# Kernel tuning notes

Measured on AMD Instinct MI355X. Metric: run time of the kernel, lower is better.

The kernel has to match this reference:

```python
import jax, jax.numpy as jnp
import numpy as np


def setup_inputs() -> dict:
    key = jax.random.key(0)
    k1, k2, k3 = jax.random.split(key, 3)
    N, K, QB = 8192, 8192, 128
    x = jax.random.normal(k1, (K,), dtype=jnp.float16)
    # packed int4 weights: two nibbles per byte, stored as int32 in [0, 256)
    packed_w = jax.random.randint(k2, (N, K // 2), 0, 256, dtype=jnp.int32)
    # per-(row, quant-block) FP16 scales, small positive values
    scales = (jax.random.uniform(k3, (N, K // QB), dtype=jnp.float32) * 0.05 + 0.001).astype(jnp.float16)
    return {"x": x, "packed_w": packed_w, "scales": scales, "qblock_size": QB}


def reference(x, packed_w, scales, qblock_size):
    # Unpack int4 weights: low nibble -> even k, high nibble -> odd k, offset-8.
    N, half_K = packed_w.shape
    K = half_K * 2
    lo = (packed_w & 0x0F) - 8          # [N, K/2]
    hi = ((packed_w >> 4) & 0x0F) - 8   # [N, K/2]
    w_int = jnp.stack([lo, hi], axis=-1).reshape(N, K).astype(jnp.float32)

    # Factored-scale GEMV (mirrors kernel: integer dot per quant-block, then one
    # multiply by the block scale).
    blocks = K // qblock_size
    wb = w_int.reshape(N, blocks, qblock_size)                 # [N, B, Q]
    xb = x.astype(jnp.float32).reshape(blocks, qblock_size)    # [B, Q]
    partial = jnp.einsum('nbq,bq->nb', wb, xb)                 # [N, B]
    out = jnp.sum(partial * scales.astype(jnp.float32), axis=1)
    return out.astype(jnp.float16)
```

## Files before the change

### kernel.cpp

```cpp
#include <hip/hip_runtime.h>


#define WAVES_PER_BLOCK 4

__global__ __launch_bounds__(256, 4)
void eoq_gemv_kernel(const float* __restrict__ x,
                     const int* __restrict__ packed_w,
                     const float* __restrict__ scales,
                     float* __restrict__ out,
                     int N, int halfK, int itMask, int sShift, int blocksPerRow)
{
    const int lane = threadIdx.x & 63;
    const int wave = threadIdx.x >> 6;
    const int row  = blockIdx.x * WAVES_PER_BLOCK + wave;
    if (row >= N) return;

    const int4*   __restrict__ w4p =
        reinterpret_cast<const int4*>(packed_w + (size_t)row * halfK);
    const float4* __restrict__ x4p = reinterpret_cast<const float4*>(x);
    const float*  __restrict__ srow = scales + (size_t)row * (size_t)blocksPerRow;

    const int iters = itMask + 1;
    const int phase = row & itMask;

    float acc = 0.f;

    #pragma unroll 4
    for (int t = 0; t < iters; ++t) {
        const int it = (t + phase) & itMask;
        const int j4 = (it << 6) + lane;
        const int4   w4 = w4p[j4];
        const float4 xa = x4p[2 * j4];
        const float4 xb = x4p[2 * j4 + 1];
        const float  s  = srow[j4 >> sShift];

        const unsigned w0 = (unsigned)w4.x;
        const unsigned w1 = (unsigned)w4.y;
        const unsigned w2 = (unsigned)w4.z;
        const unsigned w3 = (unsigned)w4.w;

        float part = 0.f;
        part = fmaf((float)(int)(w0 & 0xFu) - 8.f, xa.x, part);
        part = fmaf((float)(int)(w0 >> 4)   - 8.f, xa.y, part);
        part = fmaf((float)(int)(w1 & 0xFu) - 8.f, xa.z, part);
        part = fmaf((float)(int)(w1 >> 4)   - 8.f, xa.w, part);
        part = fmaf((float)(int)(w2 & 0xFu) - 8.f, xb.x, part);
        part = fmaf((float)(int)(w2 >> 4)   - 8.f, xb.y, part);
        part = fmaf((float)(int)(w3 & 0xFu) - 8.f, xb.z, part);
        part = fmaf((float)(int)(w3 >> 4)   - 8.f, xb.w, part);
        acc = fmaf(s, part, acc);
    }

    #pragma unroll
    for (int off = 32; off > 0; off >>= 1)
        acc += __shfl_down(acc, off, 64);

    if (lane == 0) out[row] = acc;
}

extern "C" void kernel_launch(void* const* d_in, const int* in_sizes, int n_in,
                              void* d_out, int out_size, void* d_ws, size_t ws_size,
                              hipStream_t stream) {
    const float* x      = (const float*)d_in[0];
    const int*   pw     = (const int*)d_in[1];
    const float* scales = (const float*)d_in[2];
    float*       out    = (float*)d_out;

    const int K     = in_sizes[0];
    const int halfK = K >> 1;
    const int N     = in_sizes[1] / halfK;
    const int blocksPerRow = in_sizes[2] / N;

    const int qhalf = halfK / blocksPerRow;
    int qhalfShift = 0;
    while ((1 << qhalfShift) < qhalf) ++qhalfShift;
    const int sShift = qhalfShift - 2;

    const int iters = halfK >> 8;
    const int itMask = iters - 1;

    dim3 grid((N + WAVES_PER_BLOCK - 1) / WAVES_PER_BLOCK), block(256);
    eoq_gemv_kernel<<<grid, block, 0, stream>>>(x, pw, scales, out,
                                                N, halfK, itMask, sShift, blocksPerRow);
}
```

Before: 202.5 us.

## Compute four rows per wave to reuse activation loads

Each wavefront now accumulates four output rows and shares each loaded x vector across them, using four times fewer blocks. This reduces redundant activation loads and per-row overhead and exposes more independent weight loads per iteration. In exchange, fewer waves are launched and the occupancy hint is lowered, and the per-row iteration phase stagger is dropped, which may change memory channel contention.

```diff
diff --git a/kernel.cpp b/kernel.cpp
--- a/kernel.cpp
+++ b/kernel.cpp
@@ -1,61 +1,70 @@
 #include <hip/hip_runtime.h>
 
 
-#define WAVES_PER_BLOCK 4
+#define ROWS_PER_WAVE 4
 
-__global__ __launch_bounds__(256, 4)
+__global__ __launch_bounds__(256, 2)
 void eoq_gemv_kernel(const float* __restrict__ x,
                      const int* __restrict__ packed_w,
                      const float* __restrict__ scales,
                      float* __restrict__ out,
-                     int N, int halfK, int itMask, int sShift, int blocksPerRow)
+                     int N, int halfK, int iters, int sShift, int blocksPerRow)
 {
     const int lane = threadIdx.x & 63;
     const int wave = threadIdx.x >> 6;
-    const int row  = blockIdx.x * WAVES_PER_BLOCK + wave;
-    if (row >= N) return;
+    const int row0 = (blockIdx.x * 4 + wave) * ROWS_PER_WAVE;
+    if (row0 >= N) return;
 
-    const int4*   __restrict__ w4p =
-        reinterpret_cast<const int4*>(packed_w + (size_t)row * halfK);
     const float4* __restrict__ x4p = reinterpret_cast<const float4*>(x);
-    const float*  __restrict__ srow = scales + (size_t)row * (size_t)blocksPerRow;
 
-    const int iters = itMask + 1;
-    const int phase = row & itMask;
+    const int4* w4p[ROWS_PER_WAVE];
+    const float* srow[ROWS_PER_WAVE];
+    #pragma unroll
+    for (int r = 0; r < ROWS_PER_WAVE; ++r) {
+        w4p[r]  = reinterpret_cast<const int4*>(packed_w + (size_t)(row0 + r) * halfK);
+        srow[r] = scales + (size_t)(row0 + r) * blocksPerRow;
+    }
 
-    float acc = 0.f;
+    float acc[ROWS_PER_WAVE] = {0.f, 0.f, 0.f, 0.f};
 
-    #pragma unroll 4
-    for (int t = 0; t < iters; ++t) {
-        const int it = (t + phase) & itMask;
+    #pragma unroll 2
+    for (int it = 0; it < iters; ++it) {
         const int j4 = (it << 6) + lane;
-        const int4   w4 = w4p[j4];
         const float4 xa = x4p[2 * j4];
         const float4 xb = x4p[2 * j4 + 1];
-        const float  s  = srow[j4 >> sShift];
+        const int    sIdx = j4 >> sShift;
 
-        const unsigned w0 = (unsigned)w4.x;
-        const unsigned w1 = (unsigned)w4.y;
-        const unsigned w2 = (unsigned)w4.z;
-        const unsigned w3 = (unsigned)w4.w;
+        #pragma unroll
+        for (int r = 0; r < ROWS_PER_WAVE; ++r) {
+            const int4  w4 = w4p[r][j4];
+            const float s  = srow[r][sIdx];
 
-        float part = 0.f;
-        part = fmaf((float)(int)(w0 & 0xFu) - 8.f, xa.x, part);
-        part = fmaf((float)(int)(w0 >> 4)   - 8.f, xa.y, part);
-        part = fmaf((float)(int)(w1 & 0xFu) - 8.f, xa.z, part);
-        part = fmaf((float)(int)(w1 >> 4)   - 8.f, xa.w, part);
-        part = fmaf((float)(int)(w2 & 0xFu) - 8.f, xb.x, part);
-        part = fmaf((float)(int)(w2 >> 4)   - 8.f, xb.y, part);
-        part = fmaf((float)(int)(w3 & 0xFu) - 8.f, xb.z, part);
-        part = fmaf((float)(int)(w3 >> 4)   - 8.f, xb.w, part);
-        acc = fmaf(s, part, acc);
+            const unsigned w0 = (unsigned)w4.x;
+            const unsigned w1 = (unsigned)w4.y;
+            const unsigned w2 = (unsigned)w4.z;
+            const unsigned w3 = (unsigned)w4.w;
+
+            float part = 0.f;
+            part = fmaf((float)(int)(w0 & 0xFu) - 8.f, xa.x, part);
+            part = fmaf((float)(int)(w0 >> 4)   - 8.f, xa.y, part);
+            part = fmaf((float)(int)(w1 & 0xFu) - 8.f, xa.z, part);
+            part = fmaf((float)(int)(w1 >> 4)   - 8.f, xa.w, part);
+            part = fmaf((float)(int)(w2 & 0xFu) - 8.f, xb.x, part);
+            part = fmaf((float)(int)(w2 >> 4)   - 8.f, xb.y, part);
+            part = fmaf((float)(int)(w3 & 0xFu) - 8.f, xb.z, part);
+            part = fmaf((float)(int)(w3 >> 4)   - 8.f, xb.w, part);
+            acc[r] = fmaf(s, part, acc[r]);
+        }
     }
 
     #pragma unroll
-    for (int off = 32; off > 0; off >>= 1)
-        acc += __shfl_down(acc, off, 64);
-
-    if (lane == 0) out[row] = acc;
+    for (int r = 0; r < ROWS_PER_WAVE; ++r) {
+        float a = acc[r];
+        #pragma unroll
+        for (int off = 32; off > 0; off >>= 1)
+            a += __shfl_down(a, off, 64);
+        if (lane == 0 && row0 + r < N) out[row0 + r] = a;
+    }
 }
 
 extern "C" void kernel_launch(void* const* d_in, const int* in_sizes, int n_in,
@@ -77,9 +86,9 @@
     const int sShift = qhalfShift - 2;
 
     const int iters = halfK >> 8;
-    const int itMask = iters - 1;
 
-    dim3 grid((N + WAVES_PER_BLOCK - 1) / WAVES_PER_BLOCK), block(256);
+    const int rowsPerBlock = 4 * ROWS_PER_WAVE;
+    dim3 grid((N + rowsPerBlock - 1) / rowsPerBlock), block(256);
     eoq_gemv_kernel<<<grid, block, 0, stream>>>(x, pw, scales, out,
-                                                N, halfK, itMask, sShift, blocksPerRow);
+                                                N, halfK, iters, sShift, blocksPerRow);
 }
```

After: 197.1 us. 2.7% less time.

## Software-pipeline weight/x loads with register ring buffer and shuffle-broadcast scales

Applied to the files above, without the earlier changes.

Adds a four-deep register prefetch ring so the weight and x loads for iteration t+4 are issued while iteration t is computed. Removes the per-row phase rotation of the K traversal. When a row has at most 64 scale blocks, each lane loads one scale up front and the loop broadcasts it with a wavefront shuffle instead of a global load per iteration. The prefetch buffers raise register pressure, which may cut occupancy under the existing launch bounds. Dropping the phase rotation means all rows read x in the same order, which may concentrate cache traffic.

```diff
diff --git a/kernel.cpp b/kernel.cpp
--- a/kernel.cpp
+++ b/kernel.cpp
@@ -1,38 +1,59 @@
 #include <hip/hip_runtime.h>
 
 
-#define WAVES_PER_BLOCK 4
+#define PF 4
 
+template<bool SHFL_SCALES>
 __global__ __launch_bounds__(256, 4)
 void eoq_gemv_kernel(const float* __restrict__ x,
                      const int* __restrict__ packed_w,
                      const float* __restrict__ scales,
                      float* __restrict__ out,
-                     int N, int halfK, int itMask, int sShift, int blocksPerRow)
+                     int N, int halfK, int iters, int sShift, int blocksPerRow)
 {
     const int lane = threadIdx.x & 63;
     const int wave = threadIdx.x >> 6;
-    const int row  = blockIdx.x * WAVES_PER_BLOCK + wave;
+    const int row  = blockIdx.x * 4 + wave;
     if (row >= N) return;
 
     const int4*   __restrict__ w4p =
         reinterpret_cast<const int4*>(packed_w + (size_t)row * halfK);
     const float4* __restrict__ x4p = reinterpret_cast<const float4*>(x);
-    const float*  __restrict__ srow = scales + (size_t)row * (size_t)blocksPerRow;
+    const float*  __restrict__ srow = scales + (size_t)row * blocksPerRow;
 
-    const int iters = itMask + 1;
-    const int phase = row & itMask;
+    float sAll = 0.f;
+    if (SHFL_SCALES) {
+        sAll = (lane < blocksPerRow) ? srow[lane] : 0.f;
+    }
+
+    int4   wbuf[PF];
+    float4 xabuf[PF];
+    float4 xbbuf[PF];
+
+    #pragma unroll
+    for (int p = 0; p < PF; ++p) {
+        const int c  = (p < iters) ? p : (iters - 1);
+        const int j4 = (c << 6) + lane;
+        wbuf[p]  = w4p[j4];
+        xabuf[p] = x4p[2 * j4];
+        xbbuf[p] = x4p[2 * j4 + 1];
+    }
 
     float acc = 0.f;
 
     #pragma unroll 4
     for (int t = 0; t < iters; ++t) {
-        const int it = (t + phase) & itMask;
-        const int j4 = (it << 6) + lane;
-        const int4   w4 = w4p[j4];
-        const float4 xa = x4p[2 * j4];
-        const float4 xb = x4p[2 * j4 + 1];
-        const float  s  = srow[j4 >> sShift];
+        const int slot = t & (PF - 1);
+        const int4   w4 = wbuf[slot];
+        const float4 xa = xabuf[slot];
+        const float4 xb = xbbuf[slot];
+
+        float s;
+        if (SHFL_SCALES) {
+            s = __shfl(sAll, ((t << 6) + lane) >> sShift, 64);
+        } else {
+            s = srow[((t << 6) + lane) >> sShift];
+        }
 
         const unsigned w0 = (unsigned)w4.x;
         const unsigned w1 = (unsigned)w4.y;
@@ -49,6 +70,12 @@
         part = fmaf((float)(int)(w3 & 0xFu) - 8.f, xb.z, part);
         part = fmaf((float)(int)(w3 >> 4)   - 8.f, xb.w, part);
         acc = fmaf(s, part, acc);
+
+        const int nc = (t + PF < iters) ? (t + PF) : (iters - 1);
+        const int j4 = (nc << 6) + lane;
+        wbuf[slot]  = w4p[j4];
+        xabuf[slot] = x4p[2 * j4];
+        xbbuf[slot] = x4p[2 * j4 + 1];
     }
 
     #pragma unroll
@@ -77,9 +104,13 @@
     const int sShift = qhalfShift - 2;
 
     const int iters = halfK >> 8;
-    const int itMask = iters - 1;
 
-    dim3 grid((N + WAVES_PER_BLOCK - 1) / WAVES_PER_BLOCK), block(256);
-    eoq_gemv_kernel<<<grid, block, 0, stream>>>(x, pw, scales, out,
-                                                N, halfK, itMask, sShift, blocksPerRow);
+    dim3 grid((N + 3) / 4), block(256);
+    if (blocksPerRow <= 64) {
+        eoq_gemv_kernel<true><<<grid, block, 0, stream>>>(
+            x, pw, scales, out, N, halfK, iters, sShift, blocksPerRow);
+    } else {
+        eoq_gemv_kernel<false><<<grid, block, 0, stream>>>(
+            x, pw, scales, out, N, halfK, iters, sShift, blocksPerRow);
+    }
 }
```

New measurement: 289.4 us. 1.43x slower.

## Add register-pipelined GEMV kernel with prefetch depth and shuffled scales

Applied to the files above, without the earlier changes.

Adds a templated kernel for the 16-iteration case that prefetches weights and x into an 8-deep register ring buffer, fully unrolls the loop, and loads all row scales once then distributes them via wave shuffles. The aim is to raise memory-level parallelism and hide load latency in the bandwidth-bound GEMV. It removes the per-row phase rotation and keeps a generic fallback kernel. The cost is higher register usage, which may limit occupancy.

```diff
diff --git a/kernel.cpp b/kernel.cpp
--- a/kernel.cpp
+++ b/kernel.cpp
@@ -1,33 +1,103 @@
 #include <hip/hip_runtime.h>
 
 
-#define WAVES_PER_BLOCK 4
+#define DEPTH 8
 
+template<int ITERS>
 __global__ __launch_bounds__(256, 4)
-void eoq_gemv_kernel(const float* __restrict__ x,
-                     const int* __restrict__ packed_w,
-                     const float* __restrict__ scales,
-                     float* __restrict__ out,
-                     int N, int halfK, int itMask, int sShift, int blocksPerRow)
+void eoq_gemv_pipe(const float* __restrict__ x,
+                   const int* __restrict__ packed_w,
+                   const float* __restrict__ scales,
+                   float* __restrict__ out,
+                   int N, int halfK, int sShift, int blocksPerRow)
 {
     const int lane = threadIdx.x & 63;
     const int wave = threadIdx.x >> 6;
-    const int row  = blockIdx.x * WAVES_PER_BLOCK + wave;
+    const int row  = blockIdx.x * 4 + wave;
     if (row >= N) return;
 
     const int4*   __restrict__ w4p =
         reinterpret_cast<const int4*>(packed_w + (size_t)row * halfK);
     const float4* __restrict__ x4p = reinterpret_cast<const float4*>(x);
-    const float*  __restrict__ srow = scales + (size_t)row * (size_t)blocksPerRow;
+    const float*  __restrict__ srow = scales + (size_t)row * blocksPerRow;
 
-    const int iters = itMask + 1;
-    const int phase = row & itMask;
+    const float sAll = (lane < blocksPerRow) ? srow[lane] : 0.f;
+
+    int4   wr[DEPTH];
+    float4 xar[DEPTH];
+    float4 xbr[DEPTH];
+
+    #pragma unroll
+    for (int p = 0; p < DEPTH; ++p) {
+        const int j4 = (p << 6) + lane;
+        wr[p]  = w4p[j4];
+        xar[p] = x4p[2 * j4];
+        xbr[p] = x4p[2 * j4 + 1];
+    }
 
     float acc = 0.f;
 
-    #pragma unroll 4
-    for (int t = 0; t < iters; ++t) {
-        const int it = (t + phase) & itMask;
+    #pragma unroll
+    for (int t = 0; t < ITERS; ++t) {
+        const int slot = t & (DEPTH - 1);
+
+        const int4   w4 = wr[slot];
+        const float4 xa = xar[slot];
+        const float4 xb = xbr[slot];
+
+        if (t + DEPTH < ITERS) {
+            const int j4 = ((t + DEPTH) << 6) + lane;
+            wr[slot]  = w4p[j4];
+            xar[slot] = x4p[2 * j4];
+            xbr[slot] = x4p[2 * j4 + 1];
+        }
+
+        const float s = __shfl(sAll, ((t << 6) + lane) >> sShift, 64);
+
+        const unsigned w0 = (unsigned)w4.x;
+        const unsigned w1 = (unsigned)w4.y;
+        const unsigned w2 = (unsigned)w4.z;
+        const unsigned w3 = (unsigned)w4.w;
+
+        float part = 0.f;
+        part = fmaf((float)(int)(w0 & 0xFu) - 8.f, xa.x, part);
+        part = fmaf((float)(int)(w0 >> 4)   - 8.f, xa.y, part);
+        part = fmaf((float)(int)(w1 & 0xFu) - 8.f, xa.z, part);
+        part = fmaf((float)(int)(w1 >> 4)   - 8.f, xa.w, part);
+        part = fmaf((float)(int)(w2 & 0xFu) - 8.f, xb.x, part);
+        part = fmaf((float)(int)(w2 >> 4)   - 8.f, xb.y, part);
+        part = fmaf((float)(int)(w3 & 0xFu) - 8.f, xb.z, part);
+        part = fmaf((float)(int)(w3 >> 4)   - 8.f, xb.w, part);
+        acc = fmaf(s, part, acc);
+    }
+
+    #pragma unroll
+    for (int off = 32; off > 0; off >>= 1)
+        acc += __shfl_down(acc, off, 64);
+
+    if (lane == 0) out[row] = acc;
+}
+
+__global__ __launch_bounds__(256, 2)
+void eoq_gemv_generic(const float* __restrict__ x,
+                      const int* __restrict__ packed_w,
+                      const float* __restrict__ scales,
+                      float* __restrict__ out,
+                      int N, int halfK, int iters, int sShift, int blocksPerRow)
+{
+    const int lane = threadIdx.x & 63;
+    const int wave = threadIdx.x >> 6;
+    const int row  = blockIdx.x * 4 + wave;
+    if (row >= N) return;
+
+    const int4*   __restrict__ w4p =
+        reinterpret_cast<const int4*>(packed_w + (size_t)row * halfK);
+    const float4* __restrict__ x4p = reinterpret_cast<const float4*>(x);
+    const float*  __restrict__ srow = scales + (size_t)row * blocksPerRow;
+
+    float acc = 0.f;
+    #pragma unroll 2
+    for (int it = 0; it < iters; ++it) {
         const int j4 = (it << 6) + lane;
         const int4   w4 = w4p[j4];
         const float4 xa = x4p[2 * j4];
@@ -77,9 +147,13 @@
     const int sShift = qhalfShift - 2;
 
     const int iters = halfK >> 8;
-    const int itMask = iters - 1;
 
-    dim3 grid((N + WAVES_PER_BLOCK - 1) / WAVES_PER_BLOCK), block(256);
-    eoq_gemv_kernel<<<grid, block, 0, stream>>>(x, pw, scales, out,
-                                                N, halfK, itMask, sShift, blocksPerRow);
+    dim3 grid((N + 3) / 4), block(256);
+    if (iters == 16 && blocksPerRow <= 64) {
+        eoq_gemv_pipe<16><<<grid, block, 0, stream>>>(
+            x, pw, scales, out, N, halfK, sShift, blocksPerRow);
+    } else {
+        eoq_gemv_generic<<<grid, block, 0, stream>>>(
+            x, pw, scales, out, N, halfK, iters, sShift, blocksPerRow);
+    }
 }
```

After: 198.3 us. -2.1%, faster.
